# Optimization experiments

Measured on AMD Instinct MI355X. Metric: run time of the kernel, lower is better.

Reference implementation:

```python
import jax, jax.numpy as jnp
import numpy as np

DIM = 512
CODEBOOK_SIZE = 8192


def setup_inputs() -> dict:
    key = jax.random.key(0)
    k_x, k_e = jax.random.split(key)
    x = jax.random.normal(k_x, (4, 4096, DIM), dtype=jnp.float32)
    # EuclideanCodebook buffer: embed ~ randn(codebook_size, dim)
    embed = jax.random.normal(k_e, (CODEBOOK_SIZE, DIM), dtype=jnp.float32)
    return {"x": x, "embed": embed}


def reference(x, embed):
    # projection_in / projection_out are Identity (codebook_dim=None)
    shape = x.shape
    flatten = x.reshape(-1, shape[-1])  # [N, D]
    # dist = -(||f||^2 - 2 f @ e^T + ||e||^2)  -> negative squared euclidean
    f_sq = jnp.sum(flatten * flatten, axis=1, keepdims=True)          # [N, 1]
    e_sq = jnp.sum(embed * embed, axis=1)[None, :]                    # [1, K]
    dist = -(f_sq - 2.0 * flatten @ embed.T + e_sq)                   # [N, K]
    embed_ind = jnp.argmax(dist, axis=-1)                             # [N]
    embed_ind = embed_ind.reshape(shape[:-1])                         # [B, S]
    quantize = jnp.take(embed, embed_ind, axis=0)                     # [B, S, D]
    return quantize, embed_ind
```

## Files before the change

kernel.cpp:

```cpp
#include <hip/hip_runtime.h>

#define DIM    512
#define KCODES 8192
#define NROWS  16384
#define NEG_INF -3.402823466e38f
#define MARGIN 2.0f
#define CPR 128

typedef unsigned short ushort_t;
typedef unsigned int uint_t;
typedef __attribute__((ext_vector_type(4))) int   v4i;
typedef __attribute__((ext_vector_type(4))) float v4f;

__device__ inline void dma16(const void* g, void* l) {
    __builtin_amdgcn_global_load_lds(
        (const __attribute__((address_space(1))) unsigned int*)g,
        (__attribute__((address_space(3))) unsigned int*)l, 16, 0, 0);
}

__global__ __launch_bounds__(512) void convert_kernel(
    const float* __restrict__ x, const float* __restrict__ embed,
    int4* __restrict__ e_t8, int4* __restrict__ x_t8,
    float* __restrict__ e_sq, float* __restrict__ esqh,
    float* __restrict__ f_sq,
    float* __restrict__ e_scale, float* __restrict__ f_scale)
{
    __shared__ __align__(16) char buf[64][528];

    const int w = threadIdx.x >> 6;
    const int lane = threadIdx.x & 63;
    const bool isE = blockIdx.x < (KCODES / 64);
    const int rows0 = isE ? blockIdx.x * 64 : (blockIdx.x - KCODES / 64) * 64;
    const float* src_base = isE ? embed : x;

    #pragma unroll
    for (int rr = 0; rr < 8; ++rr) {
        int r_local = w * 8 + rr;
        const float* src = src_base + (size_t)(rows0 + r_local) * DIM + lane * 8;
        float4 a = *(const float4*)src;
        float4 b = *(const float4*)(src + 4);
        float s = a.x*a.x + a.y*a.y + a.z*a.z + a.w*a.w
                + b.x*b.x + b.y*b.y + b.z*b.z + b.w*b.w;
        float am = fmaxf(fmaxf(fmaxf(fabsf(a.x), fabsf(a.y)), fmaxf(fabsf(a.z), fabsf(a.w))),
                         fmaxf(fmaxf(fabsf(b.x), fabsf(b.y)), fmaxf(fabsf(b.z), fabsf(b.w))));
        #pragma unroll
        for (int off = 32; off >= 1; off >>= 1) {
            s += __shfl_xor(s, off, 64);
            am = fmaxf(am, __shfl_xor(am, off, 64));
        }
        float inv = (am > 0.0f) ? 127.0f / am : 0.0f;

        float vq[8] = {a.x, a.y, a.z, a.w, b.x, b.y, b.z, b.w};
        uint_t lo = 0, hi = 0;
        #pragma unroll
        for (int jj = 0; jj < 4; ++jj) {
            lo |= ((uint_t)((int)rintf(vq[jj]     * inv) & 0xff)) << (8 * jj);
            hi |= ((uint_t)((int)rintf(vq[4 + jj] * inv) & 0xff)) << (8 * jj);
        }
        *(int*)&buf[r_local][8 * lane]     = (int)lo;
        *(int*)&buf[r_local][8 * lane + 4] = (int)hi;

        if (lane == 0) {
            int r = rows0 + r_local;
            float sc = am * (1.0f / 127.0f);
            if (isE) { e_sq[r] = s; esqh[r] = -0.5f * s; e_scale[r] = sc; }
            else     { f_sq[r] = s; f_scale[r] = sc; }
        }
    }
    __syncthreads();

    #pragma unroll
    for (int i = 0; i < 4; ++i) {
        int sq = w * 4 + i;
        int4 v = *(const int4*)&buf[lane][16 * sq];
        if (isE) e_t8[(size_t)sq * KCODES + rows0 + lane] = v;
        else     x_t8[(size_t)sq * NROWS  + rows0 + lane] = v;
    }
}

__global__ __launch_bounds__(512, 2) void screen_kernel(
    const int4* __restrict__ e_t8, const int4* __restrict__ x_t8,
    const float* __restrict__ esqh,
    const float* __restrict__ e_scale, const float* __restrict__ f_scale,
    float* __restrict__ cand_s, int* __restrict__ cand_i)
{
    __shared__ __align__(16) char EH[2][8][256][16];
    __shared__ __align__(16) char XH[2][8][256][16];

    const int t = threadIdx.x;
    const int w = t >> 6;
    const int lane = t & 63;
    const int quad = lane >> 4;
    const int l15 = lane & 15;
    const int wm = w & 1;
    const int wn = w >> 1;

    const int n = blockIdx.x;
    const int xcd = n & 7;
    const int j = n >> 3;
    const int rt = xcd * 8 + (j & 7);
    const int ct = j >> 3;
    const int row0 = rt * 256;
    const int cbase = ct * 256;

    const bool isE = w < 4;
    const int4* gbase = isE ? (e_t8 + cbase + w * 64 + lane)
                            : (x_t8 + row0 + (w - 4) * 64 + lane);
    const size_t gstride = isE ? KCODES : NROWS;

    v4i acc[8][4];
    #pragma unroll
    for (int mi = 0; mi < 8; ++mi)
        #pragma unroll
        for (int nj = 0; nj < 4; ++nj)
            acc[mi][nj] = (v4i){0, 0, 0, 0};

    auto issue_dma = [&](int S) {
        int buf = S & 1;
        char* ldst = isE ? &EH[buf][0][(w & 3) * 64][0] : &XH[buf][0][(w & 3) * 64][0];
        #pragma unroll
        for (int q = 0; q < 8; ++q) {
            int sq = S * 8 + q;
            dma16(gbase + (size_t)sq * gstride, ldst + q * 256 * 16);
        }
    };

    issue_dma(0);

    for (int S = 0; S < 4; ++S) {
        __syncthreads();
        if (S < 3) issue_dma(S + 1);
        const int buf = S & 1;

        #pragma unroll
        for (int ks = 0; ks < 2; ++ks) {
            const int q = ks * 4 + quad;
            v4i bh[4];
            #pragma unroll
            for (int nj = 0; nj < 4; ++nj)
                bh[nj] = *(const v4i*)(&XH[buf][q][wn * 64 + nj * 16 + l15][0]);
            #pragma unroll
            for (int mi = 0; mi < 8; ++mi) {
                v4i ah = *(const v4i*)(&EH[buf][q][wm * 128 + mi * 16 + l15][0]);
                #pragma unroll
                for (int nj = 0; nj < 4; ++nj)
                    acc[mi][nj] = __builtin_amdgcn_mfma_i32_16x16x64_i8(ah, bh[nj], acc[mi][nj], 0, 0, 0);
            }
        }
    }

    #pragma unroll
    for (int nj = 0; nj < 4; ++nj) {
        float sfv = f_scale[row0 + wn * 64 + nj * 16 + l15];
        float b1 = NEG_INF, b2 = NEG_INF;
        int   i1 = 0x7fffffff, i2 = 0x7fffffff;
        #pragma unroll
        for (int mi = 0; mi < 8; ++mi) {
            v4f se4 = *(const v4f*)(e_scale + cbase + wm * 128 + mi * 16 + quad * 4);
            v4f eq4 = *(const v4f*)(esqh    + cbase + wm * 128 + mi * 16 + quad * 4);
            int cid0 = cbase + wm * 128 + mi * 16 + quad * 4;
            #pragma unroll
            for (int jj = 0; jj < 4; ++jj) {
                float sc = fmaf(sfv * se4[jj], (float)acc[mi][nj][jj], eq4[jj]);
                int cc = cid0 + jj;
                if (sc > b1)      { b2 = b1; i2 = i1; b1 = sc; i1 = cc; }
                else if (sc > b2) { b2 = sc; i2 = cc; }
            }
        }
        #pragma unroll
        for (int o = 16; o <= 32; o <<= 1) {
            float c1 = __shfl_xor(b1, o, 64);
            int   j1 = __shfl_xor(i1, o, 64);
            float c2 = __shfl_xor(b2, o, 64);
            int   j2 = __shfl_xor(i2, o, 64);
            if (c1 > b1) {
                b2 = fmaxf(b1, c2); i2 = (b1 >= c2) ? i1 : j2;
                b1 = c1; i1 = j1;
            } else {
                i2 = (b2 >= c1) ? i2 : j1;
                b2 = fmaxf(b2, c1);
            }
        }
        if (quad == 0) {
            int row = row0 + wn * 64 + nj * 16 + l15;
            size_t b = (size_t)row * CPR + (ct * 4 + wm * 2);
            cand_s[b]     = b1;  cand_i[b]     = i1;
            cand_s[b + 1] = b2;  cand_i[b + 1] = i2;
        }
    }
}

__global__ __launch_bounds__(256) void rescore_kernel(
    const float* __restrict__ x, const float* __restrict__ embed,
    const float* __restrict__ e_sq, const float* __restrict__ f_sq,
    const float* __restrict__ cand_s, const int* __restrict__ cand_i,
    float* __restrict__ out)
{
    int row = blockIdx.x * 4 + (threadIdx.x >> 6);
    int lane = threadIdx.x & 63;
    size_t cb = (size_t)row * CPR;

    float cs0 = cand_s[cb + lane];
    float cs1 = cand_s[cb + 64 + lane];
    int   ci0 = cand_i[cb + lane];
    int   ci1 = cand_i[cb + 64 + lane];

    float m = fmaxf(cs0, cs1);
    #pragma unroll
    for (int o = 32; o >= 1; o >>= 1) m = fmaxf(m, __shfl_xor(m, o, 64));

    unsigned long long mask0 = __ballot(cs0 >= m - MARGIN);
    unsigned long long mask1 = __ballot(cs1 >= m - MARGIN);

    const float4* xsrc = (const float4*)(x + (size_t)row * DIM + lane * 8);
    float4 xa = xsrc[0], xb = xsrc[1];
    float fsq = f_sq[row];

    float bd = NEG_INF;
    int   bi = 0x7fffffff;

    #pragma unroll
    for (int s = 0; s < 2; ++s) {
        unsigned long long mask = s ? mask1 : mask0;
        while (mask) {
            int p = __ffsll(mask) - 1;
            mask &= mask - 1;
            int c = __shfl(s ? ci1 : ci0, p);
            const float4* er = (const float4*)(embed + (size_t)c * DIM + lane * 8);
            float4 ea = er[0], eb = er[1];
            float part = xa.x*ea.x + xa.y*ea.y + xa.z*ea.z + xa.w*ea.w
                       + xb.x*eb.x + xb.y*eb.y + xb.z*eb.z + xb.w*eb.w;
            #pragma unroll
            for (int o = 32; o >= 1; o >>= 1) part += __shfl_xor(part, o, 64);
            float d = -((fsq - 2.0f * part) + e_sq[c]);
            if (d > bd || (d == bd && c < bi)) { bd = d; bi = c; }
        }
    }

    const float4* er = (const float4*)(embed + (size_t)bi * DIM + lane * 8);
    float4 qa = er[0], qb = er[1];
    float4* dst = (float4*)(out + (size_t)row * DIM + lane * 8);
    dst[0] = qa; dst[1] = qb;
    if (lane == 0) out[(size_t)NROWS * DIM + row] = (float)bi;
}

extern "C" void kernel_launch(void* const* d_in, const int* in_sizes, int n_in,
                              void* d_out, int out_size, void* d_ws, size_t ws_size,
                              hipStream_t stream)
{
    const float* x     = (const float*)d_in[0];
    const float* embed = (const float*)d_in[1];
    float* out = (float*)d_out;

    float* e_sq    = (float*)d_ws;
    float* esqh    = e_sq + KCODES;
    float* f_sq    = esqh + KCODES;
    float* e_scale = f_sq + NROWS;
    float* f_scale = e_scale + KCODES;
    float* cand_s  = f_scale + NROWS;
    int*   cand_i  = (int*)(cand_s + (size_t)NROWS * CPR);
    int4*  e_t8    = (int4*)(cand_i + (size_t)NROWS * CPR);

    int4* x_t8 = (int4*)d_out;

    (void)in_sizes; (void)n_in; (void)out_size; (void)ws_size;

    convert_kernel<<<(KCODES + NROWS) / 64, 512, 0, stream>>>(
        x, embed, e_t8, x_t8, e_sq, esqh, f_sq, e_scale, f_scale);
    screen_kernel<<<2048, 512, 0, stream>>>(
        e_t8, x_t8, esqh, e_scale, f_scale, cand_s, cand_i);
    rescore_kernel<<<NROWS / 4, 256, 0, stream>>>(
        x, embed, e_sq, f_sq, cand_s, cand_i, out);
}
```

Before: 232.2 us.

## Split screen tile across 16 waves with LDS merge of per-wave top-2

The screen kernel moves from 512 to 1024 threads per block. Each wave now owns a 64x64 sub-tile instead of 128x64, which halves the accumulator registers per thread and raises the waves available to hide latency. Because each wave now sees only 64 codes, per-wave top-2 candidates are staged in LDS. Pairs of waves are then merged so the candidate layout written to global memory stays the same. This adds an extra barrier and an LDS merge pass, and launch_bounds(1024,4) may force register limits or spills.

```diff
diff --git a/kernel.cpp b/kernel.cpp
--- a/kernel.cpp
+++ b/kernel.cpp
@@ -78,7 +78,7 @@
     }
 }
 
-__global__ __launch_bounds__(512, 2) void screen_kernel(
+__global__ __launch_bounds__(1024, 4) void screen_kernel(
     const int4* __restrict__ e_t8, const int4* __restrict__ x_t8,
     const float* __restrict__ esqh,
     const float* __restrict__ e_scale, const float* __restrict__ f_scale,
@@ -92,8 +92,8 @@
     const int lane = t & 63;
     const int quad = lane >> 4;
     const int l15 = lane & 15;
-    const int wm = w & 1;
-    const int wn = w >> 1;
+    const int wm = w & 3;
+    const int wn = w >> 2;
 
     const int n = blockIdx.x;
     const int xcd = n & 7;
@@ -103,26 +103,26 @@
     const int row0 = rt * 256;
     const int cbase = ct * 256;
 
-    const bool isE = w < 4;
-    const int4* gbase = isE ? (e_t8 + cbase + w * 64 + lane)
-                            : (x_t8 + row0 + (w - 4) * 64 + lane);
+    const bool isE = w < 8;
+    const int qp = isE ? w : (w - 8);
+    const int4* gbase = isE ? (e_t8 + cbase + lane)
+                            : (x_t8 + row0 + lane);
     const size_t gstride = isE ? KCODES : NROWS;
 
-    v4i acc[8][4];
-    #pragma unroll
-    for (int mi = 0; mi < 8; ++mi)
+    v4i acc[4][4];
+    #pragma unroll
+    for (int mi = 0; mi < 4; ++mi)
         #pragma unroll
         for (int nj = 0; nj < 4; ++nj)
             acc[mi][nj] = (v4i){0, 0, 0, 0};
 
     auto issue_dma = [&](int S) {
         int buf = S & 1;
-        char* ldst = isE ? &EH[buf][0][(w & 3) * 64][0] : &XH[buf][0][(w & 3) * 64][0];
-        #pragma unroll
-        for (int q = 0; q < 8; ++q) {
-            int sq = S * 8 + q;
-            dma16(gbase + (size_t)sq * gstride, ldst + q * 256 * 16);
-        }
+        char* ldst = isE ? &EH[buf][qp][0][0] : &XH[buf][qp][0][0];
+        size_t soff = (size_t)(S * 8 + qp) * gstride;
+        #pragma unroll
+        for (int i = 0; i < 4; ++i)
+            dma16(gbase + soff + i * 64, ldst + i * 64 * 16);
     };
 
     issue_dma(0);
@@ -140,8 +140,8 @@
             for (int nj = 0; nj < 4; ++nj)
                 bh[nj] = *(const v4i*)(&XH[buf][q][wn * 64 + nj * 16 + l15][0]);
             #pragma unroll
-            for (int mi = 0; mi < 8; ++mi) {
-                v4i ah = *(const v4i*)(&EH[buf][q][wm * 128 + mi * 16 + l15][0]);
+            for (int mi = 0; mi < 4; ++mi) {
+                v4i ah = *(const v4i*)(&EH[buf][q][wm * 64 + mi * 16 + l15][0]);
                 #pragma unroll
                 for (int nj = 0; nj < 4; ++nj)
                     acc[mi][nj] = __builtin_amdgcn_mfma_i32_16x16x64_i8(ah, bh[nj], acc[mi][nj], 0, 0, 0);
@@ -149,16 +149,20 @@
         }
     }
 
+    __syncthreads();
+    float* scr_s = (float*)&EH[0][0][0][0];
+    int*   scr_i = (int*)  &XH[0][0][0][0];
+
     #pragma unroll
     for (int nj = 0; nj < 4; ++nj) {
         float sfv = f_scale[row0 + wn * 64 + nj * 16 + l15];
         float b1 = NEG_INF, b2 = NEG_INF;
         int   i1 = 0x7fffffff, i2 = 0x7fffffff;
         #pragma unroll
-        for (int mi = 0; mi < 8; ++mi) {
-            v4f se4 = *(const v4f*)(e_scale + cbase + wm * 128 + mi * 16 + quad * 4);
-            v4f eq4 = *(const v4f*)(esqh    + cbase + wm * 128 + mi * 16 + quad * 4);
-            int cid0 = cbase + wm * 128 + mi * 16 + quad * 4;
+        for (int mi = 0; mi < 4; ++mi) {
+            v4f se4 = *(const v4f*)(e_scale + cbase + wm * 64 + mi * 16 + quad * 4);
+            v4f eq4 = *(const v4f*)(esqh    + cbase + wm * 64 + mi * 16 + quad * 4);
+            int cid0 = cbase + wm * 64 + mi * 16 + quad * 4;
             #pragma unroll
             for (int jj = 0; jj < 4; ++jj) {
                 float sc = fmaf(sfv * se4[jj], (float)acc[mi][nj][jj], eq4[jj]);
@@ -182,11 +186,34 @@
             }
         }
         if (quad == 0) {
-            int row = row0 + wn * 64 + nj * 16 + l15;
-            size_t b = (size_t)row * CPR + (ct * 4 + wm * 2);
-            cand_s[b]     = b1;  cand_i[b]     = i1;
-            cand_s[b + 1] = b2;  cand_i[b + 1] = i2;
-        }
+            int rl = wn * 64 + nj * 16 + l15;
+            int base = (wm * 256 + rl) * 2;
+            scr_s[base]     = b1;  scr_i[base]     = i1;
+            scr_s[base + 1] = b2;  scr_i[base + 1] = i2;
+        }
+    }
+    __syncthreads();
+
+    if (t < 512) {
+        int rl = t >> 1;
+        int pr = t & 1;
+        int ba = ((2 * pr) * 256 + rl) * 2;
+        int bb = ((2 * pr + 1) * 256 + rl) * 2;
+        float a1 = scr_s[ba], a2 = scr_s[ba + 1];
+        int   ia = scr_i[ba], i2a = scr_i[ba + 1];
+        float c1 = scr_s[bb], c2 = scr_s[bb + 1];
+        int   ic = scr_i[bb], i2c = scr_i[bb + 1];
+        float b1, b2; int j1, j2;
+        if (a1 >= c1) {
+            b1 = a1; j1 = ia;
+            if (a2 >= c1) { b2 = a2; j2 = i2a; } else { b2 = c1; j2 = ic; }
+        } else {
+            b1 = c1; j1 = ic;
+            if (c2 >= a1) { b2 = c2; j2 = i2c; } else { b2 = a1; j2 = ia; }
+        }
+        size_t b = (size_t)(row0 + rl) * CPR + (ct * 4 + pr * 2);
+        cand_s[b]     = b1;  cand_i[b]     = j1;
+        cand_s[b + 1] = b2;  cand_i[b + 1] = j2;
     }
 }
 
@@ -267,7 +294,7 @@
 
     convert_kernel<<<(KCODES + NROWS) / 64, 512, 0, stream>>>(
         x, embed, e_t8, x_t8, e_sq, esqh, f_sq, e_scale, f_scale);
-    screen_kernel<<<2048, 512, 0, stream>>>(
+    screen_kernel<<<2048, 1024, 0, stream>>>(
         e_t8, x_t8, esqh, e_scale, f_scale, cand_s, cand_i);
     rescore_kernel<<<NROWS / 4, 256, 0, stream>>>(
         x, embed, e_sq, f_sq, cand_s, cand_i, out);
```

Result: no change. 236.3 us (+1.8%).
